# Performance work log

Hardware: AMD Instinct MI355X
Metric: run time of the kernel (lower is better)

## Reference

```python
import jax, jax.numpy as jnp
import numpy as np

# dims: B batch, T query len, S kv len (=T, self-attn prefill), D embed,
# N query heads, K kv heads, G = N//K GQA groups, H head dim
B, T, D = 2, 2048, 2048
N, K, H = 16, 4, 128
G = N // K
MIN_TS, MAX_TS = 1.0, 10000.0
W_SCALE = 0.02


def _rope(x, pos):
    # x: [B, L, heads, H]; pos: [B, L] int
    half = x.shape[-1] // 2
    frac = (2.0 * jnp.arange(half, dtype=jnp.float32)) / (2 * half)
    timescale = MIN_TS * (MAX_TS / MIN_TS) ** frac            # [half]
    sinusoid = pos[:, :, None, None].astype(jnp.float32) / timescale  # [B,L,1,half]
    sin = jnp.sin(sinusoid).astype(x.dtype)
    cos = jnp.cos(sinusoid).astype(x.dtype)
    x1, x2 = jnp.split(x, 2, axis=-1)
    return jnp.concatenate([x1 * cos - x2 * sin, x2 * cos + x1 * sin], axis=-1)


def setup_inputs() -> dict:
    key = jax.random.key(0)
    ks = jax.random.split(key, 6)
    Xq = jax.random.normal(ks[0], (B, T, D), dtype=jnp.float32)
    Xkv = jax.random.normal(ks[1], (B, T, D), dtype=jnp.float32)
    pos = jnp.tile(jnp.arange(T, dtype=jnp.int32)[None, :], (B, 1))
    Wq = jax.random.normal(ks[2], (D, N, H), dtype=jnp.float32) * W_SCALE
    Wk = jax.random.normal(ks[3], (D, K, H), dtype=jnp.float32) * W_SCALE
    Wv = jax.random.normal(ks[4], (D, K, H), dtype=jnp.float32) * W_SCALE
    Wo = jax.random.normal(ks[5], (N, H, D), dtype=jnp.float32) * W_SCALE
    return {"Xq": Xq, "Xkv": Xkv, "q_positions": pos, "kv_positions": pos,
            "Wq": Wq, "Wk": Wk, "Wv": Wv, "Wo": Wo}


def reference(Xq, Xkv, q_positions, kv_positions, Wq, Wk, Wv, Wo):
    # QKV projections (tensordot in torch == einsum over contracted axis)
    q = _rope(jnp.einsum('btd,dnh->btnh', Xq, Wq), q_positions)   # [B,T,N,H]
    k = _rope(jnp.einsum('bsd,dkh->bskh', Xkv, Wk), kv_positions)  # [B,S,K,H]
    v = jnp.einsum('bsd,dkh->bskh', Xkv, Wv)                       # [B,S,K,H]
    # GQA: query head n = kv_head*G + group (matches torch enable_gqa repeat_interleave)
    qg = q.reshape(B, T, K, G, H)
    # SDPA with explicit scale=1.0 (as in the original), causal mask
    scores = jnp.einsum('btkgh,bskh->bkgts', qg, k)                # [B,K,G,T,S]
    causal = jnp.tril(jnp.ones((T, T), dtype=bool))
    scores = jnp.where(causal, scores, jnp.finfo(scores.dtype).min)
    probs = jax.nn.softmax(scores, axis=-1)
    attn = jnp.einsum('bkgts,bskh->btkgh', probs, v).reshape(B, T, N, H)
    # o_proj contracts both (N, H) axes
    return jnp.einsum('btnh,nhd->btd', attn, Wo)
```

## Files before the change

### kernel.cpp

```cpp
#include <hip/hip_runtime.h>
#include <stdint.h>

#define Bb 2
#define Td 2048
#define Sd 2048
#define Dd 2048
#define Nh 16
#define Kvh 4
#define Hd 128

typedef unsigned short u16;
typedef short bf16x8 __attribute__((ext_vector_type(8)));
typedef float f32x4 __attribute__((ext_vector_type(4)));

__device__ __forceinline__ u16 f2bf(float f) {
  union { float f; unsigned u; } v; v.f = f;
  v.u += 0x7FFF + ((v.u >> 16) & 1);
  return (u16)(v.u >> 16);
}
__device__ __forceinline__ float bf2f(u16 h) {
  union { unsigned u; float f; } v; v.u = ((unsigned)h) << 16;
  return v.f;
}

__global__ __launch_bounds__(256) void k_convert(const float* __restrict__ in,
                                                 u16* __restrict__ out, int n8) {
  int i = blockIdx.x * 256 + threadIdx.x;
  if (i >= n8) return;
  const float4* p = (const float4*)in;
  float4 a = p[(size_t)i * 2], b = p[(size_t)i * 2 + 1];
  ushort4 r0, r1;
  r0.x = f2bf(a.x); r0.y = f2bf(a.y); r0.z = f2bf(a.z); r0.w = f2bf(a.w);
  r1.x = f2bf(b.x); r1.y = f2bf(b.y); r1.z = f2bf(b.z); r1.w = f2bf(b.w);
  ((ushort4*)out)[(size_t)i * 2] = r0;
  ((ushort4*)out)[(size_t)i * 2 + 1] = r1;
}

__global__ __launch_bounds__(256) void k_transpose_f32_bf16(const float* __restrict__ in,
                                                            u16* __restrict__ out,
                                                            int R, int C) {
  __shared__ u16 tile[32][33];
  int c0 = blockIdx.x * 32, r0 = blockIdx.y * 32;
  int tx = threadIdx.x & 31, ty = threadIdx.x >> 5;
#pragma unroll
  for (int i = 0; i < 32; i += 8)
    tile[ty + i][tx] = f2bf(in[(size_t)(r0 + ty + i) * C + c0 + tx]);
  __syncthreads();
#pragma unroll
  for (int i = 0; i < 32; i += 8)
    out[(size_t)(c0 + ty + i) * R + r0 + tx] = tile[tx][ty + i];
}

__global__ __launch_bounds__(256) void k_transpose_v(const u16* __restrict__ in,
                                                     u16* __restrict__ out) {
  __shared__ u16 tile[32][33];
  int bkh = blockIdx.z;
  int b = bkh >> 2, kh = bkh & 3;
  int h0 = blockIdx.x * 32, s0 = blockIdx.y * 32;
  int tx = threadIdx.x & 31, ty = threadIdx.x >> 5;
  const u16* ib = in + (size_t)b * Sd * (Kvh * Hd) + kh * Hd;
  u16* ob = out + (size_t)(b * Kvh + kh) * Hd * Sd;
#pragma unroll
  for (int i = 0; i < 32; i += 8)
    tile[ty + i][tx] = ib[(size_t)(s0 + ty + i) * (Kvh * Hd) + h0 + tx];
  __syncthreads();
#pragma unroll
  for (int i = 0; i < 32; i += 8)
    ob[(size_t)(h0 + ty + i) * Sd + s0 + tx] = tile[tx][ty + i];
}

__global__ __launch_bounds__(256) void k_rope_tables(const int* __restrict__ pos,
                                                     float* __restrict__ cosT,
                                                     float* __restrict__ sinT, int total) {
  int idx = blockIdx.x * 256 + threadIdx.x;
  if (idx >= total) return;
  int i = idx & 63, bt = idx >> 6;
  float p = (float)pos[bt];
  float ts = powf(10000.0f, (float)i * (1.0f / 64.0f));
  float x = p / ts;
  cosT[idx] = cosf(x);
  sinT[idx] = sinf(x);
}

__global__ __launch_bounds__(256) void k_gemm_q(const u16* __restrict__ A,
                                                const u16* __restrict__ Bt,
                                                float* __restrict__ Cq,
                                                const float* __restrict__ cosT,
                                                const float* __restrict__ sinT) {
  __shared__ u16 lA[128 * 32];
  __shared__ u16 lB[128 * 32];
  int tiles_n = (Nh * Hd) >> 7;
  int bm = blockIdx.x / tiles_n, bn = blockIdx.x % tiles_n;
  int tid = threadIdx.x;
  int lane = tid & 63, wave = tid >> 6;
  int wr = wave >> 1, wc = wave & 1;
  int e0 = tid * 8;
  int r0 = e0 >> 5, c0 = e0 & 31;
  int lr = lane & 15, hi = lane >> 4;
  int kq = hi * 8;

  const u16* gA = A + (size_t)(bm * 128 + r0) * Dd + c0;
  const u16* gB = Bt + (size_t)(bn * 128 + r0) * Dd + c0;

  f32x4 acc[4][4] = {};

  for (int k0 = 0; k0 < Dd; k0 += 32) {
    __syncthreads();
    __builtin_amdgcn_global_load_lds(
        (const __attribute__((address_space(1))) uint32_t*)(gA + k0),
        (__attribute__((address_space(3))) uint32_t*)&lA[e0], 16, 0, 0);
    __builtin_amdgcn_global_load_lds(
        (const __attribute__((address_space(1))) uint32_t*)(gA + k0 + (size_t)64 * Dd),
        (__attribute__((address_space(3))) uint32_t*)&lA[e0 + 64 * 32], 16, 0, 0);
    __builtin_amdgcn_global_load_lds(
        (const __attribute__((address_space(1))) uint32_t*)(gB + k0),
        (__attribute__((address_space(3))) uint32_t*)&lB[e0], 16, 0, 0);
    __builtin_amdgcn_global_load_lds(
        (const __attribute__((address_space(1))) uint32_t*)(gB + k0 + (size_t)64 * Dd),
        (__attribute__((address_space(3))) uint32_t*)&lB[e0 + 64 * 32], 16, 0, 0);
    __syncthreads();

    bf16x8 af[4], bfr[4];
#pragma unroll
    for (int m = 0; m < 4; ++m)
      af[m] = *(const bf16x8*)&lA[(wr * 64 + m * 16 + lr) * 32 + kq];
#pragma unroll
    for (int n = 0; n < 4; ++n) {
      int rB = (n >> 1) * 64 + wc * 32 + (n & 1) * 16 + lr;
      bfr[n] = *(const bf16x8*)&lB[rB * 32 + kq];
    }
#pragma unroll
    for (int m = 0; m < 4; ++m)
#pragma unroll
      for (int n = 0; n < 4; ++n)
        acc[m][n] = __builtin_amdgcn_mfma_f32_16x16x32_bf16(af[m], bfr[n], acc[m][n], 0, 0, 0);
  }

  int orow0 = bm * 128 + wr * 64 + hi * 4;
  int head = bn;
#pragma unroll
  for (int m = 0; m < 4; ++m)
#pragma unroll
    for (int n = 0; n < 2; ++n) {
      int i = wc * 32 + n * 16 + lr;
#pragma unroll
      for (int q = 0; q < 4; ++q) {
        int r = orow0 + m * 16 + q;
        float c = cosT[r * 64 + i], s = sinT[r * 64 + i];
        float x1 = acc[m][n][q], x2 = acc[m][n + 2][q];
        size_t base = (size_t)r * (Nh * Hd) + head * Hd;
        Cq[base + i]      = x1 * c - x2 * s;
        Cq[base + i + 64] = x2 * c + x1 * s;
      }
    }
}

__global__ __launch_bounds__(256) void k_gemm_kv(const u16* __restrict__ A,
                                                 const u16* __restrict__ Bt,
                                                 u16* __restrict__ Kb,
                                                 u16* __restrict__ Cv,
                                                 const float* __restrict__ cosT,
                                                 const float* __restrict__ sinT) {
  __shared__ u16 lA[128 * 32];
  __shared__ u16 lB[128 * 32];
  int bm = blockIdx.x >> 3, bn = blockIdx.x & 7;
  int tid = threadIdx.x;
  int lane = tid & 63, wave = tid >> 6;
  int wr = wave >> 1, wc = wave & 1;
  int e0 = tid * 8;
  int r0 = e0 >> 5, c0 = e0 & 31;
  int lr = lane & 15, hi = lane >> 4;
  int kq = hi * 8;

  const u16* gA = A + (size_t)(bm * 128 + r0) * Dd + c0;
  const u16* gB = Bt + (size_t)(bn * 128 + r0) * Dd + c0;

  f32x4 acc[4][4] = {};

  for (int k0 = 0; k0 < Dd; k0 += 32) {
    __syncthreads();
    __builtin_amdgcn_global_load_lds(
        (const __attribute__((address_space(1))) uint32_t*)(gA + k0),
        (__attribute__((address_space(3))) uint32_t*)&lA[e0], 16, 0, 0);
    __builtin_amdgcn_global_load_lds(
        (const __attribute__((address_space(1))) uint32_t*)(gA + k0 + (size_t)64 * Dd),
        (__attribute__((address_space(3))) uint32_t*)&lA[e0 + 64 * 32], 16, 0, 0);
    __builtin_amdgcn_global_load_lds(
        (const __attribute__((address_space(1))) uint32_t*)(gB + k0),
        (__attribute__((address_space(3))) uint32_t*)&lB[e0], 16, 0, 0);
    __builtin_amdgcn_global_load_lds(
        (const __attribute__((address_space(1))) uint32_t*)(gB + k0 + (size_t)64 * Dd),
        (__attribute__((address_space(3))) uint32_t*)&lB[e0 + 64 * 32], 16, 0, 0);
    __syncthreads();

    bf16x8 af[4], bfr[4];
#pragma unroll
    for (int m = 0; m < 4; ++m)
      af[m] = *(const bf16x8*)&lA[(wr * 64 + m * 16 + lr) * 32 + kq];
#pragma unroll
    for (int n = 0; n < 4; ++n) {
      int rB = (n >> 1) * 64 + wc * 32 + (n & 1) * 16 + lr;
      bfr[n] = *(const bf16x8*)&lB[rB * 32 + kq];
    }
#pragma unroll
    for (int m = 0; m < 4; ++m)
#pragma unroll
      for (int n = 0; n < 4; ++n)
        acc[m][n] = __builtin_amdgcn_mfma_f32_16x16x32_bf16(af[m], bfr[n], acc[m][n], 0, 0, 0);
  }

  int orow0 = bm * 128 + wr * 64 + hi * 4;
  if (bn < 4) {
    int kh = bn;
#pragma unroll
    for (int m = 0; m < 4; ++m)
#pragma unroll
      for (int n = 0; n < 2; ++n) {
        int i = wc * 32 + n * 16 + lr;
#pragma unroll
        for (int q = 0; q < 4; ++q) {
          int r = orow0 + m * 16 + q;
          int b = r >> 11, s = r & 2047;
          float c = cosT[r * 64 + i], sn = sinT[r * 64 + i];
          float x1 = acc[m][n][q], x2 = acc[m][n + 2][q];
          size_t base = (((size_t)(b * Kvh + kh)) * Sd + s) * Hd;
          Kb[base + i]      = f2bf(x1 * c - x2 * sn);
          Kb[base + i + 64] = f2bf(x2 * c + x1 * sn);
        }
      }
  } else {
#pragma unroll
    for (int m = 0; m < 4; ++m)
#pragma unroll
      for (int n = 0; n < 4; ++n) {
        int col = (bn - 4) * 128 + (n >> 1) * 64 + wc * 32 + (n & 1) * 16 + lr;
#pragma unroll
        for (int q = 0; q < 4; ++q)
          Cv[(size_t)(orow0 + m * 16 + q) * 512 + col] = f2bf(acc[m][n][q]);
      }
  }
}

__global__ __launch_bounds__(256) void k_gemm_bt(const u16* __restrict__ A,
                                                 const u16* __restrict__ Bt,
                                                 float* __restrict__ C,
                                                 int M, int Ncols, int Kd) {
  __shared__ u16 lA[128 * 32];
  __shared__ u16 lB[128 * 32];
  int tiles_n = Ncols >> 7;
  int bm = blockIdx.x / tiles_n, bn = blockIdx.x % tiles_n;
  int tid = threadIdx.x;
  int lane = tid & 63, wave = tid >> 6;
  int wr = wave >> 1, wc = wave & 1;
  int e0 = tid * 8;
  int r0 = e0 >> 5, c0 = e0 & 31;
  int lr = lane & 15, hi = lane >> 4;
  int kq = hi * 8;

  const u16* gA = A + (size_t)(bm * 128 + r0) * Kd + c0;
  const u16* gB = Bt + (size_t)(bn * 128 + r0) * Kd + c0;

  f32x4 acc[4][4] = {};

  for (int k0 = 0; k0 < Kd; k0 += 32) {
    __syncthreads();
    __builtin_amdgcn_global_load_lds(
        (const __attribute__((address_space(1))) uint32_t*)(gA + k0),
        (__attribute__((address_space(3))) uint32_t*)&lA[e0], 16, 0, 0);
    __builtin_amdgcn_global_load_lds(
        (const __attribute__((address_space(1))) uint32_t*)(gA + k0 + (size_t)64 * Kd),
        (__attribute__((address_space(3))) uint32_t*)&lA[e0 + 64 * 32], 16, 0, 0);
    __builtin_amdgcn_global_load_lds(
        (const __attribute__((address_space(1))) uint32_t*)(gB + k0),
        (__attribute__((address_space(3))) uint32_t*)&lB[e0], 16, 0, 0);
    __builtin_amdgcn_global_load_lds(
        (const __attribute__((address_space(1))) uint32_t*)(gB + k0 + (size_t)64 * Kd),
        (__attribute__((address_space(3))) uint32_t*)&lB[e0 + 64 * 32], 16, 0, 0);
    __syncthreads();

    bf16x8 af[4], bfr[4];
#pragma unroll
    for (int m = 0; m < 4; ++m)
      af[m] = *(const bf16x8*)&lA[(wr * 64 + m * 16 + lr) * 32 + kq];
#pragma unroll
    for (int n = 0; n < 4; ++n)
      bfr[n] = *(const bf16x8*)&lB[(wc * 64 + n * 16 + lr) * 32 + kq];
#pragma unroll
    for (int m = 0; m < 4; ++m)
#pragma unroll
      for (int n = 0; n < 4; ++n)
        acc[m][n] = __builtin_amdgcn_mfma_f32_16x16x32_bf16(af[m], bfr[n], acc[m][n], 0, 0, 0);
  }

  int orow0 = bm * 128 + wr * 64 + hi * 4;
  int ocol0 = bn * 128 + wc * 64 + lr;
#pragma unroll
  for (int m = 0; m < 4; ++m)
#pragma unroll
    for (int n = 0; n < 4; ++n)
#pragma unroll
      for (int q = 0; q < 4; ++q)
        C[(size_t)(orow0 + m * 16 + q) * Ncols + ocol0 + n * 16] = acc[m][n][q];
}

__global__ __launch_bounds__(256) void k_attn(const float* __restrict__ Qf,
                                              const u16* __restrict__ K,
                                              const u16* __restrict__ Vt,
                                              u16* __restrict__ O) {
  __shared__ u16 kv[2][16384];
  __shared__ u16 Pl[4][1024];

  int bid0 = blockIdx.x;
  int bid = (bid0 & 7) * 64 + (bid0 >> 3);
  int p = bid & 15, n = (bid >> 4) & 15, b = bid >> 8;
  int kh = n >> 2;
  int tid = threadIdx.x;
  int lane = tid & 63, wave = tid >> 6;
  int lr = lane & 15, hi = lane >> 4;
  int kq = hi * 8;

  const u16* Kbase = K + ((size_t)(b * Kvh + kh)) * Sd * Hd;
  const u16* Vbase = Vt + ((size_t)(b * Kvh + kh)) * Hd * Sd;
  u16* Pw = &Pl[wave][0];

  for (int half = 0; half < 2; ++half) {
    int tile = half ? (31 - p) : p;
    int t0 = tile * 64 + wave * 16;

    bf16x8 qhi[4], qlo[4];
    {
      const float* qrow = Qf + ((size_t)((b * Td + t0 + lr) * Nh + n)) * Hd;
#pragma unroll
      for (int kk = 0; kk < 4; ++kk) {
        float4 a = *(const float4*)(qrow + kk * 32 + kq);
        float4 c = *(const float4*)(qrow + kk * 32 + kq + 4);
        float xs[8] = {a.x, a.y, a.z, a.w, c.x, c.y, c.z, c.w};
#pragma unroll
        for (int jj = 0; jj < 8; ++jj) {
          u16 h = f2bf(xs[jj]);
          qhi[kk][jj] = (short)h;
          qlo[kk][jj] = (short)f2bf(xs[jj] - bf2f(h));
        }
      }
    }

    float m_run[4] = {-1e30f, -1e30f, -1e30f, -1e30f};
    float l_run[4] = {0.f, 0.f, 0.f, 0.f};
    f32x4 oacc[8] = {};

    int nst = tile + 1;

    auto STAGE = [&](int st, int buf) {
      int s0 = st * 64;
      char* kb = (char*)&kv[buf][0];
#pragma unroll
      for (int it = 0; it < 4; ++it) {
        int o = it * 4096 + tid * 16;
        int r = o >> 8, w = o & 255;
        const u16* src = Kbase + (size_t)(s0 + r) * Hd + ((w ^ ((r & 7) << 4)) >> 1);
        __builtin_amdgcn_global_load_lds(
            (const __attribute__((address_space(1))) uint32_t*)src,
            (__attribute__((address_space(3))) uint32_t*)(kb + o), 16, 0, 0);
      }
#pragma unroll
      for (int it = 0; it < 4; ++it) {
        int o = it * 4096 + tid * 16;
        int h = o >> 7, w = o & 127;
        const u16* src = Vbase + (size_t)h * Sd + s0 + ((w ^ ((h & 7) << 4)) >> 1);
        __builtin_amdgcn_global_load_lds(
            (const __attribute__((address_space(1))) uint32_t*)src,
            (__attribute__((address_space(3))) uint32_t*)(kb + 16384 + o), 16, 0, 0);
      }
    };

    int cur = 0;
    STAGE(0, 0);
    asm volatile("s_waitcnt vmcnt(0)" ::: "memory");
    __syncthreads();

    for (int st = 0; st < nst; ++st) {
      if (st + 1 < nst) STAGE(st + 1, cur ^ 1);
      int s0 = st * 64;
      const char* kb = (const char*)&kv[cur][0];

      f32x4 sc[4] = {};
#pragma unroll
      for (int j = 0; j < 4; ++j) {
        int r = j * 16 + lr;
        int rx = (r & 7) << 4;
#pragma unroll
        for (int kk = 0; kk < 4; ++kk) {
          bf16x8 kf = *(const bf16x8*)(kb + r * 256 + ((kk * 64 + hi * 16) ^ rx));
          sc[j] = __builtin_amdgcn_mfma_f32_16x16x32_bf16(qhi[kk], kf, sc[j], 0, 0, 0);
          sc[j] = __builtin_amdgcn_mfma_f32_16x16x32_bf16(qlo[kk], kf, sc[j], 0, 0, 0);
        }
      }

      if (s0 + 63 > t0) {
#pragma unroll
        for (int j = 0; j < 4; ++j) {
          if (s0 + j * 16 + 15 > t0) {
            int s = s0 + j * 16 + lr;
#pragma unroll
            for (int q = 0; q < 4; ++q)
              if (s > t0 + hi * 4 + q) sc[j][q] = -1e30f;
          }
        }
      }

      float mb[4], ls[4];
#pragma unroll
      for (int q = 0; q < 4; ++q)
        mb[q] = fmaxf(fmaxf(sc[0][q], sc[1][q]), fmaxf(sc[2][q], sc[3][q]));
#pragma unroll
      for (int off = 1; off < 16; off <<= 1) {
#pragma unroll
        for (int q = 0; q < 4; ++q) mb[q] = fmaxf(mb[q], __shfl_xor(mb[q], off));
      }
      bool need = (mb[0] > m_run[0] + 8.f) || (mb[1] > m_run[1] + 8.f) ||
                  (mb[2] > m_run[2] + 8.f) || (mb[3] > m_run[3] + 8.f);
      if (__any(need)) {
        float fac[4];
#pragma unroll
        for (int q = 0; q < 4; ++q) {
          float mn = fmaxf(m_run[q], mb[q]);
          fac[q] = __expf(m_run[q] - mn);
          m_run[q] = mn;
          l_run[q] *= fac[q];
        }
#pragma unroll
        for (int hb = 0; hb < 8; ++hb)
#pragma unroll
          for (int q = 0; q < 4; ++q) oacc[hb][q] *= fac[q];
      }
#pragma unroll
      for (int j = 0; j < 4; ++j)
#pragma unroll
        for (int q = 0; q < 4; ++q) sc[j][q] = __expf(sc[j][q] - m_run[q]);
#pragma unroll
      for (int q = 0; q < 4; ++q)
        ls[q] = (sc[0][q] + sc[1][q]) + (sc[2][q] + sc[3][q]);
#pragma unroll
      for (int off = 1; off < 16; off <<= 1) {
#pragma unroll
        for (int q = 0; q < 4; ++q) ls[q] += __shfl_xor(ls[q], off);
      }
#pragma unroll
      for (int q = 0; q < 4; ++q) l_run[q] += ls[q];

#pragma unroll
      for (int j = 0; j < 4; ++j)
#pragma unroll
        for (int q = 0; q < 4; ++q) {
          int row = hi * 4 + q;
          int cb = ((j * 16 + lr) * 2) ^ ((row & 7) << 4);
          *(u16*)((char*)Pw + row * 128 + cb) = f2bf(sc[j][q]);
        }
      bf16x8 pf[2];
      {
        int rx = (lr & 7) << 4;
#pragma unroll
        for (int c = 0; c < 2; ++c)
          pf[c] = *(const bf16x8*)((const char*)Pw + lr * 128 + ((c * 64 + hi * 16) ^ rx));
      }

#pragma unroll
      for (int hb = 0; hb < 8; ++hb) {
        int h = hb * 16 + lr;
        int rx = (h & 7) << 4;
#pragma unroll
        for (int c = 0; c < 2; ++c) {
          bf16x8 vf = *(const bf16x8*)(kb + 16384 + h * 128 + ((c * 64 + hi * 16) ^ rx));
          oacc[hb] = __builtin_amdgcn_mfma_f32_16x16x32_bf16(pf[c], vf, oacc[hb], 0, 0, 0);
        }
      }

      asm volatile("s_waitcnt vmcnt(0)" ::: "memory");
      __syncthreads();
      cur ^= 1;
    }

#pragma unroll
    for (int hb = 0; hb < 8; ++hb)
#pragma unroll
      for (int q = 0; q < 4; ++q) {
        float val = oacc[hb][q] / l_run[q];
        O[((size_t)((b * Td + t0 + hi * 4 + q) * Nh + n)) * Hd + hb * 16 + lr] = f2bf(val);
      }
  }
}

extern "C" void kernel_launch(void* const* d_in, const int* in_sizes, int n_in,
                              void* d_out, int out_size, void* d_ws, size_t ws_size,
                              hipStream_t stream) {
  (void)in_sizes; (void)n_in; (void)out_size; (void)ws_size;
  const float* Xq  = (const float*)d_in[0];
  const float* Xkv = (const float*)d_in[1];
  const int* qpos  = (const int*)d_in[2];
  const int* kpos  = (const int*)d_in[3];
  const float* Wq  = (const float*)d_in[4];
  const float* Wk  = (const float*)d_in[5];
  const float* Wv  = (const float*)d_in[6];
  const float* Wo  = (const float*)d_in[7];
  float* out = (float*)d_out;

  char* ws = (char*)d_ws;
  size_t off = 0;
  auto take = [&](size_t bytes) -> char* {
    char* p = ws + off;
    off += (bytes + 255) & ~(size_t)255;
    return p;
  };
  const size_t nX   = (size_t)Bb * Td * Dd;
  const size_t nQ   = (size_t)Bb * Td * Nh * Hd;
  const size_t nKV  = (size_t)Bb * Sd * Kvh * Hd;
  const size_t nTab = (size_t)Bb * Td * 64;

  u16* XqB   = (u16*)take(nX * 2);
  u16* XkvB  = (u16*)take(nX * 2);
  u16* WqT   = (u16*)take((size_t)Nh * Hd * Dd * 2);
  u16* BtKV  = (u16*)take((size_t)(Kvh * Hd * 2) * Dd * 2);
  u16* WoT   = (u16*)take((size_t)Dd * Nh * Hd * 2);
  float* Qf  = (float*)take(nQ * 4);
  u16* Kb    = (u16*)take(nKV * 2);
  u16* Vb    = (u16*)take(nKV * 2);
  float* cosQ = (float*)take(nTab * 4);
  float* sinQ = (float*)take(nTab * 4);
  float* cosK = (float*)take(nTab * 4);
  float* sinK = (float*)take(nTab * 4);
  u16* attnB = XqB;
  u16* Vt    = XkvB;

  k_convert<<<dim3((int)(nX / 8 / 256)), 256, 0, stream>>>(Xq, XqB, (int)(nX / 8));
  k_convert<<<dim3((int)(nX / 8 / 256)), 256, 0, stream>>>(Xkv, XkvB, (int)(nX / 8));
  k_transpose_f32_bf16<<<dim3((Nh * Hd) / 32, Dd / 32), 256, 0, stream>>>(Wq, WqT, Dd, Nh * Hd);
  k_transpose_f32_bf16<<<dim3((Kvh * Hd) / 32, Dd / 32), 256, 0, stream>>>(Wk, BtKV, Dd, Kvh * Hd);
  k_transpose_f32_bf16<<<dim3((Kvh * Hd) / 32, Dd / 32), 256, 0, stream>>>(
      Wv, BtKV + (size_t)512 * Dd, Dd, Kvh * Hd);
  k_transpose_f32_bf16<<<dim3(Dd / 32, (Nh * Hd) / 32), 256, 0, stream>>>(Wo, WoT, Nh * Hd, Dd);
  k_rope_tables<<<dim3((int)(nTab / 256)), 256, 0, stream>>>(qpos, cosQ, sinQ, (int)nTab);
  k_rope_tables<<<dim3((int)(nTab / 256)), 256, 0, stream>>>(kpos, cosK, sinK, (int)nTab);

  k_gemm_q<<<dim3((Bb * Td / 128) * ((Nh * Hd) / 128)), 256, 0, stream>>>(
      XqB, WqT, Qf, cosQ, sinQ);
  k_gemm_kv<<<dim3((Bb * Td / 128) * 8), 256, 0, stream>>>(
      XkvB, BtKV, Kb, Vb, cosK, sinK);

  k_transpose_v<<<dim3(Hd / 32, Sd / 32, Bb * Kvh), 256, 0, stream>>>(Vb, Vt);

  k_attn<<<dim3(Bb * Nh * 16), 256, 0, stream>>>(Qf, Kb, Vt, attnB);

  k_gemm_bt<<<dim3((Bb * Td / 128) * ((Nh * Hd) / 128)), 256, 0, stream>>>(
      attnB, WoT, out, Bb * Td, Nh * Hd, Dd);
}
```

Baseline: 292.5 us.

## Merge preprocessing launches, fuse Q and KV GEMMs, defer row-sum reduction

```diff
diff --git a/kernel.cpp b/kernel.cpp
--- a/kernel.cpp
+++ b/kernel.cpp
@@ -23,10 +23,14 @@
   return v.f;
 }
 
-__global__ __launch_bounds__(256) void k_convert(const float* __restrict__ in,
-                                                 u16* __restrict__ out, int n8) {
+__global__ __launch_bounds__(256) void k_convert2(const float* __restrict__ in1,
+                                                  const float* __restrict__ in2,
+                                                  u16* __restrict__ out1,
+                                                  u16* __restrict__ out2, int n8each) {
   int i = blockIdx.x * 256 + threadIdx.x;
-  if (i >= n8) return;
+  const float* in = in1;
+  u16* out = out1;
+  if (i >= n8each) { i -= n8each; in = in2; out = out2; }
   const float4* p = (const float4*)in;
   float4 a = p[(size_t)i * 2], b = p[(size_t)i * 2 + 1];
   ushort4 r0, r1;
@@ -36,11 +40,24 @@
   ((ushort4*)out)[(size_t)i * 2 + 1] = r1;
 }
 
-__global__ __launch_bounds__(256) void k_transpose_f32_bf16(const float* __restrict__ in,
-                                                            u16* __restrict__ out,
-                                                            int R, int C) {
+__global__ __launch_bounds__(256) void k_transpose_w(const float* __restrict__ Wq,
+                                                     const float* __restrict__ Wo,
+                                                     const float* __restrict__ Wk,
+                                                     const float* __restrict__ Wv,
+                                                     u16* __restrict__ WqT,
+                                                     u16* __restrict__ WoT,
+                                                     u16* __restrict__ BtKV) {
   __shared__ u16 tile[32][33];
+  int z = blockIdx.z;
+  const float* in;
+  u16* out;
+  int R, C;
+  if (z == 0)      { in = Wq; out = WqT; R = Dd; C = Nh * Hd; }
+  else if (z == 1) { in = Wo; out = WoT; R = Nh * Hd; C = Dd; }
+  else if (z == 2) { in = Wk; out = BtKV; R = Dd; C = Kvh * Hd; }
+  else             { in = Wv; out = BtKV + (size_t)512 * Dd; R = Dd; C = Kvh * Hd; }
   int c0 = blockIdx.x * 32, r0 = blockIdx.y * 32;
+  if (c0 >= C) return;
   int tx = threadIdx.x & 31, ty = threadIdx.x >> 5;
 #pragma unroll
   for (int i = 0; i < 32; i += 8)
@@ -69,28 +86,50 @@
     ob[(size_t)(h0 + ty + i) * Sd + s0 + tx] = tile[tx][ty + i];
 }
 
-__global__ __launch_bounds__(256) void k_rope_tables(const int* __restrict__ pos,
-                                                     float* __restrict__ cosT,
-                                                     float* __restrict__ sinT, int total) {
+__global__ __launch_bounds__(256) void k_rope_tables2(const int* __restrict__ qpos,
+                                                      const int* __restrict__ kpos,
+                                                      float* __restrict__ cosQ,
+                                                      float* __restrict__ sinQ,
+                                                      float* __restrict__ cosK,
+                                                      float* __restrict__ sinK, int nTab) {
   int idx = blockIdx.x * 256 + threadIdx.x;
-  if (idx >= total) return;
+  const int* pos = qpos;
+  float* cT = cosQ;
+  float* sT = sinQ;
+  if (idx >= nTab) { idx -= nTab; pos = kpos; cT = cosK; sT = sinK; }
   int i = idx & 63, bt = idx >> 6;
   float p = (float)pos[bt];
   float ts = powf(10000.0f, (float)i * (1.0f / 64.0f));
   float x = p / ts;
-  cosT[idx] = cosf(x);
-  sinT[idx] = sinf(x);
-}
-
-__global__ __launch_bounds__(256) void k_gemm_q(const u16* __restrict__ A,
-                                                const u16* __restrict__ Bt,
-                                                float* __restrict__ Cq,
-                                                const float* __restrict__ cosT,
-                                                const float* __restrict__ sinT) {
+  cT[idx] = cosf(x);
+  sT[idx] = sinf(x);
+}
+
+__global__ __launch_bounds__(256) void k_gemm_qkv(const u16* __restrict__ Aq,
+                                                  const u16* __restrict__ Akv,
+                                                  const u16* __restrict__ BtQ,
+                                                  const u16* __restrict__ BtKV,
+                                                  float* __restrict__ Cq,
+                                                  u16* __restrict__ Kb,
+                                                  u16* __restrict__ Cv,
+                                                  const float* __restrict__ cosQ,
+                                                  const float* __restrict__ sinQ,
+                                                  const float* __restrict__ cosK,
+                                                  const float* __restrict__ sinK) {
   __shared__ u16 lA[128 * 32];
   __shared__ u16 lB[128 * 32];
-  int tiles_n = (Nh * Hd) >> 7;
-  int bm = blockIdx.x / tiles_n, bn = blockIdx.x % tiles_n;
+  int bid = blockIdx.x;
+  int isQ = bid < 512;
+  int bm, bn;
+  const u16 *A, *Bt;
+  if (isQ) {
+    bm = bid >> 4; bn = bid & 15;
+    A = Aq; Bt = BtQ;
+  } else {
+    int k = bid - 512;
+    bm = k >> 3; bn = k & 7;
+    A = Akv; Bt = BtKV;
+  }
   int tid = threadIdx.x;
   int lane = tid & 63, wave = tid >> 6;
   int wr = wave >> 1, wc = wave & 1;
@@ -137,80 +176,24 @@
   }
 
   int orow0 = bm * 128 + wr * 64 + hi * 4;
-  int head = bn;
-#pragma unroll
-  for (int m = 0; m < 4; ++m)
-#pragma unroll
-    for (int n = 0; n < 2; ++n) {
-      int i = wc * 32 + n * 16 + lr;
-#pragma unroll
-      for (int q = 0; q < 4; ++q) {
-        int r = orow0 + m * 16 + q;
-        float c = cosT[r * 64 + i], s = sinT[r * 64 + i];
-        float x1 = acc[m][n][q], x2 = acc[m][n + 2][q];
-        size_t base = (size_t)r * (Nh * Hd) + head * Hd;
-        Cq[base + i]      = x1 * c - x2 * s;
-        Cq[base + i + 64] = x2 * c + x1 * s;
-      }
-    }
-}
-
-__global__ __launch_bounds__(256) void k_gemm_kv(const u16* __restrict__ A,
-                                                 const u16* __restrict__ Bt,
-                                                 u16* __restrict__ Kb,
-                                                 u16* __restrict__ Cv,
-                                                 const float* __restrict__ cosT,
-                                                 const float* __restrict__ sinT) {
-  __shared__ u16 lA[128 * 32];
-  __shared__ u16 lB[128 * 32];
-  int bm = blockIdx.x >> 3, bn = blockIdx.x & 7;
-  int tid = threadIdx.x;
-  int lane = tid & 63, wave = tid >> 6;
-  int wr = wave >> 1, wc = wave & 1;
-  int e0 = tid * 8;
-  int r0 = e0 >> 5, c0 = e0 & 31;
-  int lr = lane & 15, hi = lane >> 4;
-  int kq = hi * 8;
-
-  const u16* gA = A + (size_t)(bm * 128 + r0) * Dd + c0;
-  const u16* gB = Bt + (size_t)(bn * 128 + r0) * Dd + c0;
-
-  f32x4 acc[4][4] = {};
-
-  for (int k0 = 0; k0 < Dd; k0 += 32) {
-    __syncthreads();
-    __builtin_amdgcn_global_load_lds(
-        (const __attribute__((address_space(1))) uint32_t*)(gA + k0),
-        (__attribute__((address_space(3))) uint32_t*)&lA[e0], 16, 0, 0);
-    __builtin_amdgcn_global_load_lds(
-        (const __attribute__((address_space(1))) uint32_t*)(gA + k0 + (size_t)64 * Dd),
-        (__attribute__((address_space(3))) uint32_t*)&lA[e0 + 64 * 32], 16, 0, 0);
-    __builtin_amdgcn_global_load_lds(
-        (const __attribute__((address_space(1))) uint32_t*)(gB + k0),
-        (__attribute__((address_space(3))) uint32_t*)&lB[e0], 16, 0, 0);
-    __builtin_amdgcn_global_load_lds(
-        (const __attribute__((address_space(1))) uint32_t*)(gB + k0 + (size_t)64 * Dd),
-        (__attribute__((address_space(3))) uint32_t*)&lB[e0 + 64 * 32], 16, 0, 0);
-    __syncthreads();
-
-    bf16x8 af[4], bfr[4];
-#pragma unroll
-    for (int m = 0; m < 4; ++m)
-      af[m] = *(const bf16x8*)&lA[(wr * 64 + m * 16 + lr) * 32 + kq];
-#pragma unroll
-    for (int n = 0; n < 4; ++n) {
-      int rB = (n >> 1) * 64 + wc * 32 + (n & 1) * 16 + lr;
-      bfr[n] = *(const bf16x8*)&lB[rB * 32 + kq];
-    }
-#pragma unroll
-    for (int m = 0; m < 4; ++m)
-#pragma unroll
-      for (int n = 0; n < 4; ++n)
-        acc[m][n] = __builtin_amdgcn_mfma_f32_16x16x32_bf16(af[m], bfr[n], acc[m][n], 0, 0, 0);
-  }
-
-  int orow0 = bm * 128 + wr * 64 + hi * 4;
-  if (bn < 4) {
+  if (isQ) {
+    int head = bn;
+#pragma unroll
+    for (int m = 0; m < 4; ++m)
+#pragma unroll
+      for (int n = 0; n < 2; ++n) {
+        int i = wc * 32 + n * 16 + lr;
+#pragma unroll
+        for (int q = 0; q < 4; ++q) {
+          int r = orow0 + m * 16 + q;
+          float c = cosQ[r * 64 + i], s = sinQ[r * 64 + i];
+          float x1 = acc[m][n][q], x2 = acc[m][n + 2][q];
+          size_t base = (size_t)r * (Nh * Hd) + head * Hd;
+          Cq[base + i]      = x1 * c - x2 * s;
+          Cq[base + i + 64] = x2 * c + x1 * s;
+        }
+      }
+  } else if (bn < 4) {
     int kh = bn;
 #pragma unroll
     for (int m = 0; m < 4; ++m)
@@ -221,7 +204,7 @@
         for (int q = 0; q < 4; ++q) {
           int r = orow0 + m * 16 + q;
           int b = r >> 11, s = r & 2047;
-          float c = cosT[r * 64 + i], sn = sinT[r * 64 + i];
+          float c = cosK[r * 64 + i], sn = sinK[r * 64 + i];
           float x1 = acc[m][n][q], x2 = acc[m][n + 2][q];
           size_t base = (((size_t)(b * Kvh + kh)) * Sd + s) * Hd;
           Kb[base + i]      = f2bf(x1 * c - x2 * sn);
@@ -408,7 +391,7 @@
         }
       }
 
-      float mb[4], ls[4];
+      float mb[4];
 #pragma unroll
       for (int q = 0; q < 4; ++q)
         mb[q] = fmaxf(fmaxf(sc[0][q], sc[1][q]), fmaxf(sc[2][q], sc[3][q]));
@@ -439,14 +422,7 @@
         for (int q = 0; q < 4; ++q) sc[j][q] = __expf(sc[j][q] - m_run[q]);
 #pragma unroll
       for (int q = 0; q < 4; ++q)
-        ls[q] = (sc[0][q] + sc[1][q]) + (sc[2][q] + sc[3][q]);
-#pragma unroll
-      for (int off = 1; off < 16; off <<= 1) {
-#pragma unroll
-        for (int q = 0; q < 4; ++q) ls[q] += __shfl_xor(ls[q], off);
-      }
-#pragma unroll
-      for (int q = 0; q < 4; ++q) l_run[q] += ls[q];
+        l_run[q] += (sc[0][q] + sc[1][q]) + (sc[2][q] + sc[3][q]);
 
 #pragma unroll
       for (int j = 0; j < 4; ++j)
@@ -480,6 +456,11 @@
       cur ^= 1;
     }
 
+#pragma unroll
+    for (int off = 1; off < 16; off <<= 1) {
+#pragma unroll
+      for (int q = 0; q < 4; ++q) l_run[q] += __shfl_xor(l_run[q], off);
+    }
 #pragma unroll
     for (int hb = 0; hb < 8; ++hb)
 #pragma unroll
@@ -531,20 +512,14 @@
   u16* attnB = XqB;
   u16* Vt    = XkvB;
 
-  k_convert<<<dim3((int)(nX / 8 / 256)), 256, 0, stream>>>(Xq, XqB, (int)(nX / 8));
-  k_convert<<<dim3((int)(nX / 8 / 256)), 256, 0, stream>>>(Xkv, XkvB, (int)(nX / 8));
-  k_transpose_f32_bf16<<<dim3((Nh * Hd) / 32, Dd / 32), 256, 0, stream>>>(Wq, WqT, Dd, Nh * Hd);
-  k_transpose_f32_bf16<<<dim3((Kvh * Hd) / 32, Dd / 32), 256, 0, stream>>>(Wk, BtKV, Dd, Kvh * Hd);
-  k_transpose_f32_bf16<<<dim3((Kvh * Hd) / 32, Dd / 32), 256, 0, stream>>>(
-      Wv, BtKV + (size_t)512 * Dd, Dd, Kvh * Hd);
-  k_transpose_f32_bf16<<<dim3(Dd / 32, (Nh * Hd) / 32), 256, 0, stream>>>(Wo, WoT, Nh * Hd, Dd);
-  k_rope_tables<<<dim3((int)(nTab / 256)), 256, 0, stream>>>(qpos, cosQ, sinQ, (int)nTab);
-  k_rope_tables<<<dim3((int)(nTab / 256)), 256, 0, stream>>>(kpos, cosK, sinK, (int)nTab);
-
-  k_gemm_q<<<dim3((Bb * Td / 128) * ((Nh * Hd) / 128)), 256, 0, stream>>>(
-      XqB, WqT, Qf, cosQ, sinQ);
-  k_gemm_kv<<<dim3((Bb * Td / 128) * 8), 256, 0, stream>>>(
-      XkvB, BtKV, Kb, Vb, cosK, sinK);
+  k_convert2<<<dim3((int)(2 * nX / 8 / 256)), 256, 0, stream>>>(
+      Xq, Xkv, XqB, XkvB, (int)(nX / 8));
+  k_transpose_w<<<dim3(64, 64, 4), 256, 0, stream>>>(Wq, Wo, Wk, Wv, WqT, WoT, BtKV);
+  k_rope_tables2<<<dim3((int)(2 * nTab / 256)), 256, 0, stream>>>(
+      qpos, kpos, cosQ, sinQ, cosK, sinK, (int)nTab);
+
+  k_gemm_qkv<<<dim3(512 + 256), 256, 0, stream>>>(
+      XqB, XkvB, WqT, BtKV, Qf, Kb, Vb, cosQ, sinQ, cosK, sinK);
 
   k_transpose_v<<<dim3(Hd / 32, Sd / 32, Bb * Kvh), 256, 0, stream>>>(Vb, Vt);
 
```

New measurement: 319.3 us. 9.2% more time.
